# Optimization experiments

Measured on AMD Instinct MI355X. Metric: run time of the kernel, lower is better.

Reference implementation:

```python
import jax, jax.numpy as jnp
import numpy as np

N, LD, LM, D = 8, 1024, 1024, 1024
H = 16
HS = D // H  # 64

def setup_inputs() -> dict:
    key = jax.random.key(0)
    k1, k2, k3 = jax.random.split(key, 3)
    inp = jax.random.normal(k1, (N, LD, D), dtype=jnp.float32)
    mem = jax.random.normal(k2, (N, LM, D), dtype=jnp.float32)
    mask = jnp.ones((N, LM), dtype=jnp.float32)
    Wc = jax.random.normal(k3, (D, 2 * D), dtype=jnp.float32) * 0.02
    bc = jnp.zeros((D,), dtype=jnp.float32)
    return {"input": inp, "memory": mem, "mask": mask, "Wc": Wc, "bc": bc}

def reference(input, memory, mask, Wc, bc):
    # split heads: [N, L, D] -> [N, H, L, HS]
    q = input.reshape(N, LD, H, HS).transpose(0, 2, 1, 3)
    k = memory.reshape(N, LM, H, HS).transpose(0, 2, 1, 3)
    v = k
    scores = jnp.einsum('bhqd,bhkd->bhqk', q, k) / jnp.sqrt(jnp.float32(HS))
    # additive key-padding mask: -1e30 * (1 - mask), broadcast over heads & queries
    scores = scores + (-1e30) * (1.0 - mask[:, None, None, :])
    probs = jax.nn.softmax(scores, axis=-1)
    ctx = jnp.einsum('bhqk,bhkd->bhqd', probs, v)
    ctx = ctx.transpose(0, 2, 1, 3).reshape(N, LD, D)
    out = jnp.concatenate([input, ctx], axis=-1) @ Wc.T + bc
    return jax.nn.sigmoid(out) * jnp.tanh(out)
```

## Files before the change

kernel.cpp:

```cpp
#include <hip/hip_runtime.h>

#define NB 8
#define LSEQ 1024
#define DMODEL 1024
#define NH 16
#define HS 64
#define KX 2048

typedef __bf16 bf16_t;
typedef __attribute__((ext_vector_type(4))) __bf16 bf16x4;
typedef __attribute__((ext_vector_type(8))) __bf16 bf16x8;
typedef __attribute__((ext_vector_type(4))) float floatx4;

typedef __attribute__((address_space(3))) unsigned int lds_u32;
typedef const __attribute__((address_space(1))) unsigned int glob_u32;

__device__ __forceinline__ floatx4 mfma16(bf16x8 a, bf16x8 b, floatx4 c) {
    return __builtin_amdgcn_mfma_f32_16x16x32_bf16(a, b, c, 0, 0, 0);
}
__device__ __forceinline__ void gl_lds16(const bf16_t* g, bf16_t* l) {
    __builtin_amdgcn_global_load_lds((glob_u32*)g, (lds_u32*)l, 16, 0, 0);
}

__global__ __launch_bounds__(256) void convert_kernel(
        const float* __restrict__ inp, const float* __restrict__ mem,
        const float* __restrict__ Wc,
        bf16_t* __restrict__ Xb, bf16_t* __restrict__ Mb, bf16_t* __restrict__ Wb) {
    const size_t RA = 1048576, RB = 2097152;
    size_t t = (size_t)blockIdx.x * 256 + threadIdx.x;
    const float* src;
    bf16_t* dst;
    if (t < RA) {
        size_t i8 = t * 8;
        src = inp + i8;
        dst = Xb + (i8 >> 10) * 2048 + (i8 & 1023);
    } else if (t < RB) {
        size_t i8 = (t - RA) * 8;
        src = mem + i8;
        dst = Mb + i8;
    } else {
        size_t i8 = (t - RB) * 8;
        src = Wc + i8;
        dst = Wb + i8;
    }
    floatx4 f0 = *(const floatx4*)(src);
    floatx4 f1 = *(const floatx4*)(src + 4);
    bf16x8 w;
#pragma unroll
    for (int j = 0; j < 4; ++j) { w[j] = (bf16_t)f0[j]; w[4 + j] = (bf16_t)f1[j]; }
    *(bf16x8*)dst = w;
}

__global__ __launch_bounds__(256) void transpose_kernel(
        const float* __restrict__ mem, bf16_t* __restrict__ VTg) {
    __shared__ bf16_t Tl[64][72];
    const int tid = threadIdx.x;
    const int bid = blockIdx.x;
    const int kb = bid & 15;
    const int h  = (bid >> 4) & 15;
    const int n  = bid >> 8;
    {
        const int key = tid >> 2, seg = tid & 3;
        const float* src = mem + ((size_t)(n * LSEQ + kb * 64 + key)) * DMODEL + h * HS + seg * 16;
        floatx4 f[4];
#pragma unroll
        for (int j = 0; j < 4; ++j) f[j] = *(const floatx4*)(src + j * 4);
        bf16_t* d = &Tl[key][seg * 16];
#pragma unroll
        for (int j = 0; j < 16; ++j) d[j] = (bf16_t)f[j >> 2][j & 3];
    }
    __syncthreads();
    {
        const int dim = tid >> 2, ks = tid & 3;
        bf16x8 w0, w1;
#pragma unroll
        for (int j = 0; j < 8; ++j) { w0[j] = Tl[ks * 16 + j][dim]; w1[j] = Tl[ks * 16 + 8 + j][dim]; }
        bf16_t* dst = VTg + ((size_t)((n * NH + h) * HS + dim)) * LSEQ + kb * 64 + ks * 16;
        *(bf16x8*)dst = w0;
        *(bf16x8*)(dst + 8) = w1;
    }
}

__global__ __launch_bounds__(256) void attn_kernel(
        bf16_t* __restrict__ Xb, const bf16_t* __restrict__ Mb,
        const bf16_t* __restrict__ VTg, const float* __restrict__ mask) {
    __shared__ __align__(16) bf16_t Kl[128 * 64];
    __shared__ __align__(16) bf16_t Vl[64 * 128];
    __shared__ __align__(16) bf16_t Pl[4 * 32 * 64];
    __shared__ float biasL[LSEQ];

    const int tid  = threadIdx.x;
    const int lane = tid & 63;
    const int wv   = tid >> 6;
    const int ln15 = lane & 15;
    const int quad = lane >> 4;

    const int bid = blockIdx.x;
    const int qt  = bid & 7;
    const int h   = (bid >> 3) & 15;
    const int n   = bid >> 7;
    const int q0  = qt * 128 + wv * 32;

    {
        const int i = tid * 4;
        floatx4 mv = *(const floatx4*)(mask + n * LSEQ + i);
#pragma unroll
        for (int j = 0; j < 4; ++j) biasL[i + j] = -1e30f * (1.0f - mv[j]) - 8.0f;
    }

    bf16x8 qf[2][2];
#pragma unroll
    for (int nt = 0; nt < 2; ++nt) {
        const bf16_t* qp = Xb + ((size_t)(n * LSEQ + q0 + nt * 16 + ln15)) * KX + h * HS;
#pragma unroll
        for (int kk = 0; kk < 2; ++kk) {
            bf16x8 r = *(const bf16x8*)(qp + kk * 32 + quad * 8);
            bf16x8 a;
#pragma unroll
            for (int j = 0; j < 8; ++j) a[j] = (bf16_t)((float)r[j] * 0.125f);
            qf[nt][kk] = a;
        }
    }

    floatx4 ot[4][2];
#pragma unroll
    for (int md = 0; md < 4; ++md)
#pragma unroll
        for (int nt = 0; nt < 2; ++nt) ot[md][nt] = (floatx4){0.f, 0.f, 0.f, 0.f};
    float lsum[2] = {0.f, 0.f};

    bf16_t* myP = &Pl[wv * 32 * 64];

    for (int kt = 0; kt < LSEQ / 128; ++kt) {
        const int kb = kt * 128;
        __syncthreads();
#pragma unroll
        for (int i = 0; i < 4; ++i) {
            const int kbase = wv * 32 + i * 8;
            const int key = kbase + (lane >> 3), s = lane & 7, g = s ^ (key & 7);
            gl_lds16(Mb + ((size_t)(n * LSEQ + kb + key)) * DMODEL + h * HS + g * 8,
                     &Kl[kbase * 64]);
        }
#pragma unroll
        for (int i = 0; i < 4; ++i) {
            const int dbase = wv * 16 + i * 4;
            const int dim = dbase + (lane >> 4), s = lane & 15, g = s ^ (dim & 7);
            gl_lds16(VTg + ((size_t)((n * NH + h) * HS + dim)) * LSEQ + kb + g * 8,
                     &Vl[dbase * 128]);
        }
        __syncthreads();

#pragma unroll
        for (int half = 0; half < 2; ++half) {
            floatx4 s4[4][2];
#pragma unroll
            for (int m = 0; m < 4; ++m) {
                const int key = half * 64 + m * 16 + ln15;
                floatx4 b4 = *(const floatx4*)(&biasL[kb + half * 64 + m * 16 + quad * 4]);
#pragma unroll
                for (int nt = 0; nt < 2; ++nt) s4[m][nt] = b4;
#pragma unroll
                for (int kk = 0; kk < 2; ++kk) {
                    const int slot = (kk * 4 + quad) ^ (ln15 & 7);
                    bf16x8 a = *(const bf16x8*)(&Kl[key * 64 + slot * 8]);
#pragma unroll
                    for (int nt = 0; nt < 2; ++nt) s4[m][nt] = mfma16(a, qf[nt][kk], s4[m][nt]);
                }
            }
#pragma unroll
            for (int m = 0; m < 4; ++m)
#pragma unroll
                for (int nt = 0; nt < 2; ++nt)
#pragma unroll
                    for (int reg = 0; reg < 4; ++reg) {
                        const float e = __expf(s4[m][nt][reg]);
                        s4[m][nt][reg] = e;
                        lsum[nt] += e;
                    }

#pragma unroll
            for (int m = 0; m < 4; ++m)
#pragma unroll
                for (int nt = 0; nt < 2; ++nt) {
                    const int q = nt * 16 + ln15;
                    const int t = m * 2 + (quad >> 1);
                    bf16x4 p;
#pragma unroll
                    for (int reg = 0; reg < 4; ++reg) p[reg] = (bf16_t)s4[m][nt][reg];
                    *(bf16x4*)(&myP[q * 64 + ((t ^ (q & 7)) * 8 + (quad & 1) * 4)]) = p;
                }
#pragma unroll
            for (int kk = 0; kk < 2; ++kk) {
                bf16x8 pb[2];
#pragma unroll
                for (int nt = 0; nt < 2; ++nt) {
                    const int q = nt * 16 + ln15;
                    const int slot = (kk * 4 + quad) ^ (q & 7);
                    pb[nt] = *(const bf16x8*)(&myP[q * 64 + slot * 8]);
                }
#pragma unroll
                for (int md = 0; md < 4; ++md) {
                    const int d = md * 16 + ln15;
                    const int vslot = (half * 8 + kk * 4 + quad) ^ (d & 7);
                    bf16x8 va = *(const bf16x8*)(&Vl[d * 128 + vslot * 8]);
#pragma unroll
                    for (int nt = 0; nt < 2; ++nt) ot[md][nt] = mfma16(va, pb[nt], ot[md][nt]);
                }
            }
        }
    }

#pragma unroll
    for (int nt = 0; nt < 2; ++nt) {
        float t = lsum[nt];
        t += __shfl_xor(t, 16);
        t += __shfl_xor(t, 32);
        const float inv = 1.0f / t;
        const int q = q0 + nt * 16 + ln15;
        bf16_t* op = Xb + ((size_t)(n * LSEQ + q)) * KX + DMODEL + h * HS;
#pragma unroll
        for (int md = 0; md < 4; ++md) {
            bf16x4 w;
#pragma unroll
            for (int reg = 0; reg < 4; ++reg) w[reg] = (bf16_t)(ot[md][nt][reg] * inv);
            *(bf16x4*)(op + md * 16 + quad * 4) = w;
        }
    }
}

__global__ __launch_bounds__(256, 4) void gemm_kernel(
        const bf16_t* __restrict__ Xb, const bf16_t* __restrict__ Wb,
        const float* __restrict__ bc, float* __restrict__ out) {
    __shared__ __align__(16) bf16_t Al[128 * 64];
    __shared__ __align__(16) bf16_t Bl[64 * 64];

    const int tid  = threadIdx.x;
    const int lane = tid & 63;
    const int wv   = tid >> 6;
    const int ln15 = lane & 15;
    const int quad = lane >> 4;

    const int bn = blockIdx.x & 15;
    const int bm = blockIdx.x >> 4;
    const int mbase = bm * 128, nbase = bn * 64;

    floatx4 acc[2][4];
#pragma unroll
    for (int i = 0; i < 2; ++i)
#pragma unroll
        for (int j = 0; j < 4; ++j) acc[i][j] = (floatx4){0.f, 0.f, 0.f, 0.f};

    for (int it = 0; it < KX / 64; ++it) {
        const int k0 = it * 64;
        __syncthreads();
#pragma unroll
        for (int i = 0; i < 4; ++i) {
            const int r0  = i * 32 + wv * 8;
            const int row = r0 + (lane >> 3);
            const int g   = (lane & 7) ^ (row & 7);
            gl_lds16(Xb + (size_t)(mbase + row) * KX + k0 + g * 8, &Al[r0 * 64]);
        }
#pragma unroll
        for (int j = 0; j < 2; ++j) {
            const int r0  = j * 32 + wv * 8;
            const int row = r0 + (lane >> 3);
            const int g   = (lane & 7) ^ (row & 7);
            gl_lds16(Wb + (size_t)(nbase + row) * KX + k0 + g * 8, &Bl[r0 * 64]);
        }
        __syncthreads();

#pragma unroll
        for (int kk = 0; kk < 2; ++kk) {
            bf16x8 af[2], bfr[4];
#pragma unroll
            for (int mi = 0; mi < 2; ++mi) {
                const int row = wv * 32 + mi * 16 + ln15;
                const int slot = (kk * 4 + quad) ^ (row & 7);
                af[mi] = *(const bf16x8*)(&Al[row * 64 + slot * 8]);
            }
#pragma unroll
            for (int ni = 0; ni < 4; ++ni) {
                const int row = ni * 16 + ln15;
                const int slot = (kk * 4 + quad) ^ (row & 7);
                bfr[ni] = *(const bf16x8*)(&Bl[row * 64 + slot * 8]);
            }
#pragma unroll
            for (int mi = 0; mi < 2; ++mi)
#pragma unroll
                for (int ni = 0; ni < 4; ++ni)
                    acc[mi][ni] = mfma16(af[mi], bfr[ni], acc[mi][ni]);
        }
    }

#pragma unroll
    for (int ni = 0; ni < 4; ++ni) {
        const int col = nbase + ni * 16 + ln15;
        const float b = bc[col];
#pragma unroll
        for (int mi = 0; mi < 2; ++mi) {
#pragma unroll
            for (int reg = 0; reg < 4; ++reg) {
                const int row = mbase + wv * 32 + mi * 16 + quad * 4 + reg;
                const float z  = acc[mi][ni][reg] + b;
                const float sg = 1.0f / (1.0f + __expf(-z));
                const float th = 2.0f / (1.0f + __expf(-2.0f * z)) - 1.0f;
                out[(size_t)row * 1024 + col] = sg * th;
            }
        }
    }
}

extern "C" void kernel_launch(void* const* d_in, const int* in_sizes, int n_in,
                              void* d_out, int out_size, void* d_ws, size_t ws_size,
                              hipStream_t stream) {
    const float* inp  = (const float*)d_in[0];
    const float* mem  = (const float*)d_in[1];
    const float* mask = (const float*)d_in[2];
    const float* Wc   = (const float*)d_in[3];
    const float* bc   = (const float*)d_in[4];
    float* out = (float*)d_out;

    bf16_t* Xb  = (bf16_t*)d_ws;
    bf16_t* Mb  = Xb + (size_t)8192 * 2048;
    bf16_t* Wb  = Mb + (size_t)8192 * 1024;
    bf16_t* VTg = Wb + (size_t)1024 * 2048;

    convert_kernel<<<9216, 256, 0, stream>>>(inp, mem, Wc, Xb, Mb, Wb);
    transpose_kernel<<<2048, 256, 0, stream>>>(mem, VTg);
    attn_kernel<<<NB * NH * (LSEQ / 128), 256, 0, stream>>>(Xb, Mb, VTg, mask);
    gemm_kernel<<<(8192 / 128) * (1024 / 64), 256, 0, stream>>>(Xb, Wb, bc, out);
}
```

Before: 233.9 us.

## Fuse prep kernels, use exp2 softmax, shrink P buffer, double-buffer GEMM

The convert and transpose kernels become one prep kernel. It reads memory once to write both the bf16 copy and the transposed V, and it precomputes the mask bias in global memory. The attention kernel folds log2(e) into the Q scale and the bias, uses exp2 directly, stages P through a smaller per-wave LDS buffer in 32-key chunks, and sets occupancy to 4 blocks. The GEMM now double-buffers its LDS tiles so the next tile's load overlaps MFMA work, at the cost of twice the LDS and a lower occupancy bound of 3.

Measured after the change: 277.3 us. 1.19x slower.

```diff
diff --git a/kernel.cpp b/kernel.cpp
--- a/kernel.cpp
+++ b/kernel.cpp
@@ -7,6 +7,8 @@
 #define HS 64
 #define KX 2048
 
+#define LOG2E 1.44269504f
+
 typedef __bf16 bf16_t;
 typedef __attribute__((ext_vector_type(4))) __bf16 bf16x4;
 typedef __attribute__((ext_vector_type(8))) __bf16 bf16x8;
@@ -22,72 +24,77 @@
     __builtin_amdgcn_global_load_lds((glob_u32*)g, (lds_u32*)l, 16, 0, 0);
 }
 
-__global__ __launch_bounds__(256) void convert_kernel(
+__global__ __launch_bounds__(256) void prep_kernel(
         const float* __restrict__ inp, const float* __restrict__ mem,
-        const float* __restrict__ Wc,
-        bf16_t* __restrict__ Xb, bf16_t* __restrict__ Mb, bf16_t* __restrict__ Wb) {
-    const size_t RA = 1048576, RB = 2097152;
-    size_t t = (size_t)blockIdx.x * 256 + threadIdx.x;
-    const float* src;
-    bf16_t* dst;
-    if (t < RA) {
-        size_t i8 = t * 8;
-        src = inp + i8;
-        dst = Xb + (i8 >> 10) * 2048 + (i8 & 1023);
-    } else if (t < RB) {
-        size_t i8 = (t - RA) * 8;
-        src = mem + i8;
-        dst = Mb + i8;
-    } else {
-        size_t i8 = (t - RB) * 8;
-        src = Wc + i8;
-        dst = Wb + i8;
-    }
-    floatx4 f0 = *(const floatx4*)(src);
-    floatx4 f1 = *(const floatx4*)(src + 4);
-    bf16x8 w;
-#pragma unroll
-    for (int j = 0; j < 4; ++j) { w[j] = (bf16_t)f0[j]; w[4 + j] = (bf16_t)f1[j]; }
-    *(bf16x8*)dst = w;
-}
-
-__global__ __launch_bounds__(256) void transpose_kernel(
-        const float* __restrict__ mem, bf16_t* __restrict__ VTg) {
+        const float* __restrict__ Wc, const float* __restrict__ mask,
+        bf16_t* __restrict__ Xb, bf16_t* __restrict__ Mb,
+        bf16_t* __restrict__ Wb, bf16_t* __restrict__ VTg,
+        float* __restrict__ biasG) {
     __shared__ bf16_t Tl[64][72];
     const int tid = threadIdx.x;
-    const int bid = blockIdx.x;
-    const int kb = bid & 15;
-    const int h  = (bid >> 4) & 15;
-    const int n  = bid >> 8;
-    {
-        const int key = tid >> 2, seg = tid & 3;
-        const float* src = mem + ((size_t)(n * LSEQ + kb * 64 + key)) * DMODEL + h * HS + seg * 16;
-        floatx4 f[4];
-#pragma unroll
-        for (int j = 0; j < 4; ++j) f[j] = *(const floatx4*)(src + j * 4);
-        bf16_t* d = &Tl[key][seg * 16];
-#pragma unroll
-        for (int j = 0; j < 16; ++j) d[j] = (bf16_t)f[j >> 2][j & 3];
-    }
-    __syncthreads();
-    {
-        const int dim = tid >> 2, ks = tid & 3;
-        bf16x8 w0, w1;
-#pragma unroll
-        for (int j = 0; j < 8; ++j) { w0[j] = Tl[ks * 16 + j][dim]; w1[j] = Tl[ks * 16 + 8 + j][dim]; }
-        bf16_t* dst = VTg + ((size_t)((n * NH + h) * HS + dim)) * LSEQ + kb * 64 + ks * 16;
-        *(bf16x8*)dst = w0;
-        *(bf16x8*)(dst + 8) = w1;
-    }
-}
-
-__global__ __launch_bounds__(256) void attn_kernel(
+    const int b = blockIdx.x;
+    if (b < 2048) {
+        const int kb = b & 15;
+        const int h  = (b >> 4) & 15;
+        const int n  = b >> 8;
+        {
+            const int key = tid >> 2, seg = tid & 3;
+            const float* src = mem + ((size_t)(n * LSEQ + kb * 64 + key)) * DMODEL + h * HS + seg * 16;
+            floatx4 f[4];
+#pragma unroll
+            for (int j = 0; j < 4; ++j) f[j] = *(const floatx4*)(src + j * 4);
+            bf16x8 w0, w1;
+#pragma unroll
+            for (int j = 0; j < 8; ++j) { w0[j] = (bf16_t)f[j >> 2][j & 3]; w1[j] = (bf16_t)f[2 + (j >> 2)][j & 3]; }
+            bf16_t* d = &Tl[key][seg * 16];
+            *(bf16x8*)d = w0;
+            *(bf16x8*)(d + 8) = w1;
+            bf16_t* md = Mb + ((size_t)(n * LSEQ + kb * 64 + key)) * DMODEL + h * HS + seg * 16;
+            *(bf16x8*)md = w0;
+            *(bf16x8*)(md + 8) = w1;
+        }
+        __syncthreads();
+        {
+            const int dim = tid >> 2, ks = tid & 3;
+            bf16x8 w0, w1;
+#pragma unroll
+            for (int j = 0; j < 8; ++j) { w0[j] = Tl[ks * 16 + j][dim]; w1[j] = Tl[ks * 16 + 8 + j][dim]; }
+            bf16_t* dst = VTg + ((size_t)((n * NH + h) * HS + dim)) * LSEQ + kb * 64 + ks * 16;
+            *(bf16x8*)dst = w0;
+            *(bf16x8*)(dst + 8) = w1;
+        }
+    } else if (b < 6144) {
+        const size_t i8 = ((size_t)(b - 2048) * 256 + tid) * 8;
+        floatx4 f0 = *(const floatx4*)(inp + i8);
+        floatx4 f1 = *(const floatx4*)(inp + i8 + 4);
+        bf16x8 w;
+#pragma unroll
+        for (int j = 0; j < 4; ++j) { w[j] = (bf16_t)f0[j]; w[4 + j] = (bf16_t)f1[j]; }
+        *(bf16x8*)(Xb + (i8 >> 10) * KX + (i8 & 1023)) = w;
+    } else if (b < 7168) {
+        const size_t i8 = ((size_t)(b - 6144) * 256 + tid) * 8;
+        floatx4 f0 = *(const floatx4*)(Wc + i8);
+        floatx4 f1 = *(const floatx4*)(Wc + i8 + 4);
+        bf16x8 w;
+#pragma unroll
+        for (int j = 0; j < 4; ++j) { w[j] = (bf16_t)f0[j]; w[4 + j] = (bf16_t)f1[j]; }
+        *(bf16x8*)(Wb + i8) = w;
+    } else {
+        const size_t i4 = ((size_t)(b - 7168) * 256 + tid) * 4;
+        floatx4 mv = *(const floatx4*)(mask + i4);
+        floatx4 o;
+#pragma unroll
+        for (int j = 0; j < 4; ++j) o[j] = (-1e30f * (1.0f - mv[j]) - 8.0f) * LOG2E;
+        *(floatx4*)(biasG + i4) = o;
+    }
+}
+
+__global__ __launch_bounds__(256, 4) void attn_kernel(
         bf16_t* __restrict__ Xb, const bf16_t* __restrict__ Mb,
-        const bf16_t* __restrict__ VTg, const float* __restrict__ mask) {
+        const bf16_t* __restrict__ VTg, const float* __restrict__ biasG) {
     __shared__ __align__(16) bf16_t Kl[128 * 64];
     __shared__ __align__(16) bf16_t Vl[64 * 128];
-    __shared__ __align__(16) bf16_t Pl[4 * 32 * 64];
-    __shared__ float biasL[LSEQ];
+    __shared__ __align__(16) bf16_t Pl[4 * 1024];
 
     const int tid  = threadIdx.x;
     const int lane = tid & 63;
@@ -101,13 +108,6 @@
     const int n   = bid >> 7;
     const int q0  = qt * 128 + wv * 32;
 
-    {
-        const int i = tid * 4;
-        floatx4 mv = *(const floatx4*)(mask + n * LSEQ + i);
-#pragma unroll
-        for (int j = 0; j < 4; ++j) biasL[i + j] = -1e30f * (1.0f - mv[j]) - 8.0f;
-    }
-
     bf16x8 qf[2][2];
 #pragma unroll
     for (int nt = 0; nt < 2; ++nt) {
@@ -117,7 +117,7 @@
             bf16x8 r = *(const bf16x8*)(qp + kk * 32 + quad * 8);
             bf16x8 a;
 #pragma unroll
-            for (int j = 0; j < 8; ++j) a[j] = (bf16_t)((float)r[j] * 0.125f);
+            for (int j = 0; j < 8; ++j) a[j] = (bf16_t)((float)r[j] * (0.125f * LOG2E));
             qf[nt][kk] = a;
         }
     }
@@ -129,7 +129,8 @@
         for (int nt = 0; nt < 2; ++nt) ot[md][nt] = (floatx4){0.f, 0.f, 0.f, 0.f};
     float lsum[2] = {0.f, 0.f};
 
-    bf16_t* myP = &Pl[wv * 32 * 64];
+    bf16_t* myP = &Pl[wv * 1024];
+    const int qm = ln15 & 6;
 
     for (int kt = 0; kt < LSEQ / 128; ++kt) {
         const int kb = kt * 128;
@@ -156,7 +157,7 @@
 #pragma unroll
             for (int m = 0; m < 4; ++m) {
                 const int key = half * 64 + m * 16 + ln15;
-                floatx4 b4 = *(const floatx4*)(&biasL[kb + half * 64 + m * 16 + quad * 4]);
+                floatx4 b4 = *(const floatx4*)(biasG + n * LSEQ + kb + half * 64 + m * 16 + quad * 4);
 #pragma unroll
                 for (int nt = 0; nt < 2; ++nt) s4[m][nt] = b4;
 #pragma unroll
@@ -173,35 +174,38 @@
                 for (int nt = 0; nt < 2; ++nt)
 #pragma unroll
                     for (int reg = 0; reg < 4; ++reg) {
-                        const float e = __expf(s4[m][nt][reg]);
+                        const float e = __builtin_amdgcn_exp2f(s4[m][nt][reg]);
                         s4[m][nt][reg] = e;
                         lsum[nt] += e;
                     }
 
 #pragma unroll
-            for (int m = 0; m < 4; ++m)
+            for (int c = 0; c < 2; ++c) {
+#pragma unroll
+                for (int mm = 0; mm < 2; ++mm) {
+                    const int m = c * 2 + mm;
+                    const int gsl = ((mm * 4 + quad) ^ qm) * 4;
+#pragma unroll
+                    for (int nt = 0; nt < 2; ++nt) {
+                        const int q = nt * 16 + ln15;
+                        bf16x4 p;
+#pragma unroll
+                        for (int reg = 0; reg < 4; ++reg) p[reg] = (bf16_t)s4[m][nt][reg];
+                        *(bf16x4*)(&myP[q * 32 + gsl]) = p;
+                    }
+                }
+                const int cglob = half * 2 + c;
+                bf16x8 pb[2];
 #pragma unroll
                 for (int nt = 0; nt < 2; ++nt) {
                     const int q = nt * 16 + ln15;
-                    const int t = m * 2 + (quad >> 1);
-                    bf16x4 p;
-#pragma unroll
-                    for (int reg = 0; reg < 4; ++reg) p[reg] = (bf16_t)s4[m][nt][reg];
-                    *(bf16x4*)(&myP[q * 64 + ((t ^ (q & 7)) * 8 + (quad & 1) * 4)]) = p;
-                }
-#pragma unroll
-            for (int kk = 0; kk < 2; ++kk) {
-                bf16x8 pb[2];
-#pragma unroll
-                for (int nt = 0; nt < 2; ++nt) {
-                    const int q = nt * 16 + ln15;
-                    const int slot = (kk * 4 + quad) ^ (q & 7);
-                    pb[nt] = *(const bf16x8*)(&myP[q * 64 + slot * 8]);
+                    const int s16 = quad ^ (qm >> 1);
+                    pb[nt] = *(const bf16x8*)(&myP[q * 32 + s16 * 8]);
                 }
 #pragma unroll
                 for (int md = 0; md < 4; ++md) {
                     const int d = md * 16 + ln15;
-                    const int vslot = (half * 8 + kk * 4 + quad) ^ (d & 7);
+                    const int vslot = (cglob * 4 + quad) ^ (d & 7);
                     bf16x8 va = *(const bf16x8*)(&Vl[d * 128 + vslot * 8]);
 #pragma unroll
                     for (int nt = 0; nt < 2; ++nt) ot[md][nt] = mfma16(va, pb[nt], ot[md][nt]);
@@ -228,11 +232,11 @@
     }
 }
 
-__global__ __launch_bounds__(256, 4) void gemm_kernel(
+__global__ __launch_bounds__(256, 3) void gemm_kernel(
         const bf16_t* __restrict__ Xb, const bf16_t* __restrict__ Wb,
         const float* __restrict__ bc, float* __restrict__ out) {
-    __shared__ __align__(16) bf16_t Al[128 * 64];
-    __shared__ __align__(16) bf16_t Bl[64 * 64];
+    __shared__ __align__(16) bf16_t Al[2][128 * 64];
+    __shared__ __align__(16) bf16_t Bl[2][64 * 64];
 
     const int tid  = threadIdx.x;
     const int lane = tid & 63;
@@ -244,30 +248,50 @@
     const int bm = blockIdx.x >> 4;
     const int mbase = bm * 128, nbase = bn * 64;
 
+    const int arow8 = lane >> 3;
+    const int ag    = (lane & 7);
+
     floatx4 acc[2][4];
 #pragma unroll
     for (int i = 0; i < 2; ++i)
 #pragma unroll
         for (int j = 0; j < 4; ++j) acc[i][j] = (floatx4){0.f, 0.f, 0.f, 0.f};
 
+#pragma unroll
+    for (int i = 0; i < 4; ++i) {
+        const int r0  = i * 32 + wv * 8;
+        const int row = r0 + arow8;
+        const int g   = ag ^ (row & 7);
+        gl_lds16(Xb + (size_t)(mbase + row) * KX + g * 8, &Al[0][r0 * 64]);
+    }
+#pragma unroll
+    for (int j = 0; j < 2; ++j) {
+        const int r0  = j * 32 + wv * 8;
+        const int row = r0 + arow8;
+        const int g   = ag ^ (row & 7);
+        gl_lds16(Wb + (size_t)(nbase + row) * KX + g * 8, &Bl[0][r0 * 64]);
+    }
+    __syncthreads();
+
     for (int it = 0; it < KX / 64; ++it) {
-        const int k0 = it * 64;
-        __syncthreads();
-#pragma unroll
-        for (int i = 0; i < 4; ++i) {
-            const int r0  = i * 32 + wv * 8;
-            const int row = r0 + (lane >> 3);
-            const int g   = (lane & 7) ^ (row & 7);
-            gl_lds16(Xb + (size_t)(mbase + row) * KX + k0 + g * 8, &Al[r0 * 64]);
-        }
-#pragma unroll
-        for (int j = 0; j < 2; ++j) {
-            const int r0  = j * 32 + wv * 8;
-            const int row = r0 + (lane >> 3);
-            const int g   = (lane & 7) ^ (row & 7);
-            gl_lds16(Wb + (size_t)(nbase + row) * KX + k0 + g * 8, &Bl[r0 * 64]);
-        }
-        __syncthreads();
+        const int cur = it & 1;
+        if (it < KX / 64 - 1) {
+            const int k1 = (it + 1) * 64;
+#pragma unroll
+            for (int i = 0; i < 4; ++i) {
+                const int r0  = i * 32 + wv * 8;
+                const int row = r0 + arow8;
+                const int g   = ag ^ (row & 7);
+                gl_lds16(Xb + (size_t)(mbase + row) * KX + k1 + g * 8, &Al[cur ^ 1][r0 * 64]);
+            }
+#pragma unroll
+            for (int j = 0; j < 2; ++j) {
+                const int r0  = j * 32 + wv * 8;
+                const int row = r0 + arow8;
+                const int g   = ag ^ (row & 7);
+                gl_lds16(Wb + (size_t)(nbase + row) * KX + k1 + g * 8, &Bl[cur ^ 1][r0 * 64]);
+            }
+        }
 
 #pragma unroll
         for (int kk = 0; kk < 2; ++kk) {
@@ -276,13 +300,13 @@
             for (int mi = 0; mi < 2; ++mi) {
                 const int row = wv * 32 + mi * 16 + ln15;
                 const int slot = (kk * 4 + quad) ^ (row & 7);
-                af[mi] = *(const bf16x8*)(&Al[row * 64 + slot * 8]);
+                af[mi] = *(const bf16x8*)(&Al[cur][row * 64 + slot * 8]);
             }
 #pragma unroll
             for (int ni = 0; ni < 4; ++ni) {
                 const int row = ni * 16 + ln15;
                 const int slot = (kk * 4 + quad) ^ (row & 7);
-                bfr[ni] = *(const bf16x8*)(&Bl[row * 64 + slot * 8]);
+                bfr[ni] = *(const bf16x8*)(&Bl[cur][row * 64 + slot * 8]);
             }
 #pragma unroll
             for (int mi = 0; mi < 2; ++mi)
@@ -290,6 +314,7 @@
                 for (int ni = 0; ni < 4; ++ni)
                     acc[mi][ni] = mfma16(af[mi], bfr[ni], acc[mi][ni]);
         }
+        __syncthreads();
     }
 
 #pragma unroll
@@ -324,9 +349,9 @@
     bf16_t* Mb  = Xb + (size_t)8192 * 2048;
     bf16_t* Wb  = Mb + (size_t)8192 * 1024;
     bf16_t* VTg = Wb + (size_t)1024 * 2048;
-
-    convert_kernel<<<9216, 256, 0, stream>>>(inp, mem, Wc, Xb, Mb, Wb);
-    transpose_kernel<<<2048, 256, 0, stream>>>(mem, VTg);
-    attn_kernel<<<NB * NH * (LSEQ / 128), 256, 0, stream>>>(Xb, Mb, VTg, mask);
+    float* biasG = (float*)(VTg + (size_t)8192 * 1024);
+
+    prep_kernel<<<7176, 256, 0, stream>>>(inp, mem, Wc, mask, Xb, Mb, Wb, VTg, biasG);
+    attn_kernel<<<NB * NH * (LSEQ / 128), 256, 0, stream>>>(Xb, Mb, VTg, biasG);
     gemm_kernel<<<(8192 / 128) * (1024 / 64), 256, 0, stream>>>(Xb, Wb, bc, out);
 }
```
